# Performance work log

Measured on AMD Instinct MI355X. Metric: run time of the kernel, lower is better.

## Reference

```python
import jax, jax.numpy as jnp
import numpy as np

WS = 8      # window_size
C = 60      # channels
EXP = 2     # exp_ratio
DEPTH = 2   # 1 + shared_depth
B, H, W = 4, 256, 256
BN_EPS = 1e-5


def setup_inputs() -> dict:
    key = jax.random.key(0)
    ks = jax.random.split(key, 15)
    def rn(k, shape, s=0.1):
        return jax.random.normal(k, shape, jnp.float32) * s
    Ce = C * EXP
    return {
        "x": jax.random.normal(ks[0], (B, C, H, W), jnp.float32),
        "lfe_w0": rn(ks[1], (DEPTH, Ce, C)),
        "lfe_b0": rn(ks[2], (DEPTH, Ce)),
        "lfe_w1": rn(ks[3], (DEPTH, C, Ce)),
        "lfe_b1": rn(ks[4], (DEPTH, C)),
        "pi_w": rn(ks[5], (DEPTH, C, C)),
        "pi_b": rn(ks[6], (DEPTH, C)),
        "bn_g": 1.0 + rn(ks[7], (DEPTH, C)),
        "bn_b": rn(ks[8], (DEPTH, C)),
        "bn_m": rn(ks[9], (DEPTH, C)),
        "bn_v": jax.random.uniform(ks[10], (DEPTH, C), jnp.float32, 0.5, 1.5),
        "mask_w": rn(ks[11], (DEPTH, C, C)),
        "mask_b": rn(ks[12], (DEPTH, C)),
        "po_w": rn(ks[13], (DEPTH, C, C)),
        "po_b": rn(ks[14], (DEPTH, C)),
    }


def _conv1x1(x, w, b):
    # x: (b,c,h,w), w: (o,c)
    return jnp.einsum('oc,bchw->bohw', w, x) + b[None, :, None, None]


def _shift(x):
    # Faithful to ShiftConv2d1: depthwise 3x3 with one-hot kernels, zero pad=1.
    c = x.shape[1]; g = c // 5
    xp = jnp.pad(x, ((0, 0), (0, 0), (1, 1), (1, 1)))
    return jnp.concatenate([
        xp[:, 0 * g:1 * g, 1:-1, 2:],    # kernel (1,2): in[i, j+1]
        xp[:, 1 * g:2 * g, 1:-1, :-2],   # kernel (1,0): in[i, j-1]
        xp[:, 2 * g:3 * g, 2:, 1:-1],    # kernel (2,1): in[i+1, j]
        xp[:, 3 * g:4 * g, :-2, 1:-1],   # kernel (0,1): in[i-1, j]
        x[:, 4 * g:],                    # kernel (1,1): identity
    ], axis=1)


def _lfe(x, w0, b0, w1, b1):
    y = _conv1x1(_shift(x), w0, b0)
    y = jax.nn.gelu(y, approximate=False)  # torch nn.GELU() is exact erf
    return _conv1x1(_shift(y), w1, b1)


def _wsa(x, pi_w, pi_b, g, bt, m, v, mw, mb, pw, pb):
    b, c, h, w = x.shape; ws = WS
    # project_inp: 1x1 conv + BatchNorm2d (eval-mode stats)
    t = _conv1x1(x, pi_w, pi_b)
    scale = (g / jnp.sqrt(v + BN_EPS))
    t = (t - m[None, :, None, None]) * scale[None, :, None, None] + bt[None, :, None, None]
    # seq_refl_win_pad (forward): pad right/bottom by ws, then copy the
    # preceding ws-wide band into the padded region (rows first, then cols).
    xp = jnp.pad(t, ((0, 0), (0, 0), (0, ws), (0, ws)))
    xp = xp.at[:, :, -ws:, :].set(xp[:, :, -2 * ws:-ws, :])
    xp = xp.at[:, :, :, -ws:].set(xp[:, :, :, -2 * ws:-ws])
    nh, nw = h // ws, w // ws
    R = (jnp.arange(nh) * ws)[:, None] + jnp.arange(2 * ws)   # (nh, 2ws)
    Cc = (jnp.arange(nw) * ws)[:, None] + jnp.arange(2 * ws)  # (nw, 2ws)
    win = xp[:, :, R[:, None, :, None], Cc[None, :, None, :]]  # (b,c,nh,nw,2ws,2ws)
    # torch .unfold(3,..).unfold(2,..) yields window axes ordered (W-dir, H-dir)
    win = jnp.swapaxes(win, -1, -2)
    # 1x1 conv stride 2 == subsample every other pixel then 1x1 conv
    sub = win[..., ::2, ::2]  # (b,c,nh,nw,ws,ws)
    q = jnp.einsum('oc,bcijpq->bijpqo', mw, sub) + mb          # (b,nh,nw,ws,ws,c)
    q = q.reshape(b * nh * nw, ws * ws, c)
    vv = t.reshape(b, c, nh, ws, nw, ws).transpose(0, 2, 4, 3, 5, 1)
    vv = vv.reshape(b * nh * nw, ws * ws, c)
    atn = jax.nn.softmax(jnp.einsum('npc,nqc->npq', q, q), axis=-1)
    y = jnp.einsum('npq,nqc->npc', atn, vv)
    y = y.reshape(b, nh, nw, ws, ws, c).transpose(0, 5, 1, 3, 2, 4).reshape(b, c, h, w)
    return _conv1x1(y, pw, pb)


def reference(x, lfe_w0, lfe_b0, lfe_w1, lfe_b1, pi_w, pi_b, bn_g, bn_b, bn_m, bn_v, mask_w, mask_b, po_w, po_b):
    for i in range(DEPTH):
        x = _lfe(x, lfe_w0[i], lfe_b0[i], lfe_w1[i], lfe_b1[i]) + x
        x = _wsa(x, pi_w[i], pi_b[i], bn_g[i], bn_b[i], bn_m[i], bn_v[i],
                 mask_w[i], mask_b[i], po_w[i], po_b[i]) + x
    return x
```

## Files before the change

kernel.cpp:

```cpp
#include <hip/hip_runtime.h>
#include <math.h>

#define Hh 256
#define Ww 256
#define HW 65536
#define Bn 4
#define Cdim 60
#define Ce 120
#define NPIX (Bn*HW)

typedef const float* fp;

__device__ __forceinline__ float gelu_exact(float x){
  return 0.5f*x*(1.f + erff(x*0.70710678118654752f));
}

__device__ __forceinline__ void tile_decode(int blk, int& b, int& h, int& tw){
  b = blk >> 10; int rem = blk & 1023; h = rem >> 2; tw = (rem & 3) << 6;
}

__global__ __launch_bounds__(256) void k_lfe1(const float* __restrict__ X, float* __restrict__ Y1,
                                              fp w0, fp b0){
  __shared__ __align__(16) float A[60*64];
  __shared__ __align__(16) float Wt[60*60];
  int tid = threadIdx.x;
  int b, h, tw; tile_decode(blockIdx.x, b, h, tw);
  const float* Xb = X + (size_t)b*(Cdim*HW);
  for (int idx = tid; idx < 60*64; idx += 256){
    int k = idx >> 6, p = idx & 63;
    int grp = k / 12;
    int hh = h, ww = tw + p; bool ok = true;
    if (grp == 0){ ww += 1; ok = (ww < Ww); }
    else if (grp == 1){ ww -= 1; ok = (ww >= 0); }
    else if (grp == 2){ hh = h+1; ok = (hh < Hh); }
    else if (grp == 3){ hh = h-1; ok = (hh >= 0); }
    A[idx] = ok ? Xb[k*HW + hh*Ww + ww] : 0.f;
  }
  for (int idx = tid; idx < 60*60; idx += 256){
    int o = idx / 60, k = idx - o*60;
    Wt[k*60 + o] = w0[idx];
  }
  __syncthreads();

  int p0 = (tid & 15)*4;
  int o0 = (tid >> 4)*4;

  #pragma unroll 1
  for (int half = 0; half < 2; half++){
    if (tid < 240){
      float acc[4][4];
      #pragma unroll
      for (int oi = 0; oi < 4; oi++){
        float bb = b0[half*60 + o0 + oi];
        #pragma unroll
        for (int pi = 0; pi < 4; pi++) acc[oi][pi] = bb;
      }
      #pragma unroll 4
      for (int k = 0; k < 60; k++){
        float4 a4 = *(const float4*)(&A[k*64 + p0]);
        float av[4] = {a4.x,a4.y,a4.z,a4.w};
        float4 w4 = *(const float4*)(&Wt[k*60 + o0]);
        float wv[4] = {w4.x,w4.y,w4.z,w4.w};
        #pragma unroll
        for (int oi = 0; oi < 4; oi++){
          #pragma unroll
          for (int pi = 0; pi < 4; pi++)
            acc[oi][pi] += wv[oi]*av[pi];
        }
      }
      float* Yb = Y1 + (size_t)b*(Ce*HW) + h*Ww + tw + p0;
      #pragma unroll
      for (int oi = 0; oi < 4; oi++){
        int o = half*60 + o0 + oi;
        float4 r;
        r.x = gelu_exact(acc[oi][0]); r.y = gelu_exact(acc[oi][1]);
        r.z = gelu_exact(acc[oi][2]); r.w = gelu_exact(acc[oi][3]);
        *(float4*)(Yb + (size_t)o*HW) = r;
      }
    }
    if (half == 0){
      __syncthreads();
      for (int idx = tid; idx < 60*60; idx += 256){
        int o = idx / 60, k = idx - o*60;
        Wt[k*60 + o] = w0[3600 + idx];
      }
      __syncthreads();
    }
  }
}

__global__ __launch_bounds__(256) void k_lfe2(const float* __restrict__ Y1,
                                              const float* __restrict__ R,
                                              float* __restrict__ X,
                                              fp w1, fp b1){
  __shared__ __align__(16) float A[60*64];
  __shared__ __align__(16) float Wt[60*68];
  int tid = threadIdx.x;
  int b, h, tw; tile_decode(blockIdx.x, b, h, tw);
  const float* Yb = Y1 + (size_t)b*(Ce*HW);
  int p0 = (tid & 15)*4;
  int o0 = (tid >> 4)*4;
  float acc[4][4];
  #pragma unroll
  for (int oi = 0; oi < 4; oi++)
    #pragma unroll
    for (int pi = 0; pi < 4; pi++) acc[oi][pi] = 0.f;

  #pragma unroll 1
  for (int half = 0; half < 2; half++){
    if (half) __syncthreads();
    for (int idx = tid; idx < 60*64; idx += 256){
      int k = idx >> 6, p = idx & 63;
      int e = half*60 + k;
      int grp = e / 24;
      int hh = h, ww = tw + p; bool ok = true;
      if (grp == 0){ ww += 1; ok = (ww < Ww); }
      else if (grp == 1){ ww -= 1; ok = (ww >= 0); }
      else if (grp == 2){ hh = h+1; ok = (hh < Hh); }
      else if (grp == 3){ hh = h-1; ok = (hh >= 0); }
      A[idx] = ok ? Yb[e*HW + hh*Ww + ww] : 0.f;
    }
    for (int idx = tid; idx < 60*60; idx += 256){
      int c = idx / 60, e = idx - c*60;
      Wt[e*68 + c] = w1[c*120 + half*60 + e];
    }
    __syncthreads();
    if (tid < 240){
      #pragma unroll 4
      for (int k = 0; k < 60; k++){
        float4 a4 = *(const float4*)(&A[k*64 + p0]);
        float av[4] = {a4.x,a4.y,a4.z,a4.w};
        float4 w4 = *(const float4*)(&Wt[k*68 + o0]);
        float wv[4] = {w4.x,w4.y,w4.z,w4.w};
        #pragma unroll
        for (int oi = 0; oi < 4; oi++){
          #pragma unroll
          for (int pi = 0; pi < 4; pi++)
            acc[oi][pi] += wv[oi]*av[pi];
        }
      }
    }
  }
  if (tid < 240){
    const float* Rp = R + (size_t)b*(Cdim*HW) + h*Ww + tw + p0;
    float* Xp = X + (size_t)b*(Cdim*HW) + h*Ww + tw + p0;
    #pragma unroll
    for (int oi = 0; oi < 4; oi++){
      int o = o0 + oi;
      float bb = b1[o];
      float4 r4 = *(const float4*)(Rp + (size_t)o*HW);
      float4 out;
      out.x = acc[oi][0] + bb + r4.x;
      out.y = acc[oi][1] + bb + r4.y;
      out.z = acc[oi][2] + bb + r4.z;
      out.w = acc[oi][3] + bb + r4.w;
      *(float4*)(Xp + (size_t)o*HW) = out;
    }
  }
}

__global__ __launch_bounds__(256) void k_wsat(const float* __restrict__ X, float* __restrict__ T,
                                              fp piw, fp pib, fp g, fp bt, fp m, fp v){
  __shared__ __align__(16) float A[60*64];
  __shared__ __align__(16) float Wt[60*68];
  int tid = threadIdx.x;
  int b, h, tw; tile_decode(blockIdx.x, b, h, tw);
  const float* Xb = X + (size_t)b*(Cdim*HW) + h*Ww + tw;
  for (int idx = tid; idx < 60*64; idx += 256){
    int k = idx >> 6, p = idx & 63;
    A[idx] = Xb[k*HW + p];
  }
  for (int idx = tid; idx < 60*60; idx += 256){
    int o = idx / 60, k = idx - o*60;
    float scale = g[o] * rsqrtf(v[o] + 1e-5f);
    Wt[k*68 + o] = piw[idx] * scale;
  }
  __syncthreads();
  if (tid < 240){
    int p0 = (tid & 15)*4;
    int o0 = (tid >> 4)*4;
    float acc[4][4];
    #pragma unroll
    for (int oi = 0; oi < 4; oi++)
      #pragma unroll
      for (int pi = 0; pi < 4; pi++) acc[oi][pi] = 0.f;
    #pragma unroll 4
    for (int k = 0; k < 60; k++){
      float4 a4 = *(const float4*)(&A[k*64 + p0]);
      float av[4] = {a4.x,a4.y,a4.z,a4.w};
      float4 w4 = *(const float4*)(&Wt[k*68 + o0]);
      float wv[4] = {w4.x,w4.y,w4.z,w4.w};
      #pragma unroll
      for (int oi = 0; oi < 4; oi++){
        #pragma unroll
        for (int pi = 0; pi < 4; pi++)
          acc[oi][pi] += wv[oi]*av[pi];
      }
    }
    float* Tb = T + (size_t)b*(Cdim*HW) + h*Ww + tw + p0;
    #pragma unroll
    for (int oi = 0; oi < 4; oi++){
      int o = o0 + oi;
      float scale = g[o] * rsqrtf(v[o] + 1e-5f);
      float cns   = (pib[o] - m[o])*scale + bt[o];
      float4 out;
      out.x = acc[oi][0] + cns;
      out.y = acc[oi][1] + cns;
      out.z = acc[oi][2] + cns;
      out.w = acc[oi][3] + cns;
      *(float4*)(Tb + (size_t)o*HW) = out;
    }
  }
}

__global__ __launch_bounds__(256) void k_attn(const float* __restrict__ T, float* __restrict__ Y,
                                              fp mw, fp mb){
  __shared__ __align__(16) float R1[64*68];
  __shared__ __align__(16) float R2[64*68];
  __shared__ __align__(16) float R3[60*64];
  int tid = threadIdx.x;
  int blk = blockIdx.x;
  int b = blk >> 10; int ij = blk & 1023; int wi = ij >> 5; int wj = ij & 31;
  const float* Tb = T + (size_t)b*(Cdim*HW);

  for (int idx = tid; idx < Cdim*64; idx += 256){
    int k = idx >> 6, p = idx & 63;
    int u = p >> 3, vq = p & 7;
    int r  = wi*8 + 2*vq; if (r > 255) r -= 8;
    int cc = wj*8 + 2*u;  if (cc > 255) cc -= 8;
    R1[k*68 + p] = Tb[k*HW + r*Ww + cc];
  }
  for (int idx = tid; idx < Cdim*Cdim; idx += 256){
    int c = idx / Cdim, k = idx - c*Cdim;
    R2[c*61 + k] = mw[idx];
  }
  __syncthreads();

  if (tid < 240){
    int p0 = (tid & 15)*4, c0 = (tid >> 4)*4;
    float4 mb4 = *(const float4*)(mb + c0);
    float bias[4] = {mb4.x, mb4.y, mb4.z, mb4.w};
    float acc[4][4];
    #pragma unroll
    for (int ci = 0; ci < 4; ci++)
      #pragma unroll
      for (int pi = 0; pi < 4; pi++) acc[ci][pi] = bias[ci];
    #pragma unroll 4
    for (int k = 0; k < Cdim; k++){
      float4 a4 = *(const float4*)(&R1[k*68 + p0]);
      float av[4] = {a4.x, a4.y, a4.z, a4.w};
      #pragma unroll
      for (int ci = 0; ci < 4; ci++){
        float wv = R2[(c0+ci)*61 + k];
        #pragma unroll
        for (int pi = 0; pi < 4; pi++)
          acc[ci][pi] += wv*av[pi];
      }
    }
    #pragma unroll
    for (int ci = 0; ci < 4; ci++)
      *(float4*)(&R3[(c0+ci)*64 + p0]) = make_float4(acc[ci][0], acc[ci][1], acc[ci][2], acc[ci][3]);
  }
  __syncthreads();

  {
    int p = tid & 63; int cg = tid >> 6;
    int pr = p >> 3, pc = p & 7;
    const float* base = Tb + (wi*8+pr)*Ww + (wj*8+pc);
    #pragma unroll
    for (int t2 = 0; t2 < 15; t2++)
      R1[p*68 + cg*15 + t2] = base[(cg*15+t2)*HW];
  }
  if (tid < 64){
    R1[tid*68 + 60] = 0.f; R1[tid*68 + 61] = 0.f;
    R1[tid*68 + 62] = 0.f; R1[tid*68 + 63] = 0.f;
  }
  {
    int p0 = (tid & 15)*4, q0 = (tid >> 4)*4;
    float acc[4][4];
    #pragma unroll
    for (int qi = 0; qi < 4; qi++)
      #pragma unroll
      for (int pi = 0; pi < 4; pi++) acc[qi][pi] = 0.f;
    #pragma unroll 4
    for (int c = 0; c < Cdim; c++){
      float4 A4 = *(const float4*)(&R3[c*64 + p0]);
      float4 B4 = *(const float4*)(&R3[c*64 + q0]);
      float Af[4] = {A4.x, A4.y, A4.z, A4.w};
      float Bf[4] = {B4.x, B4.y, B4.z, B4.w};
      #pragma unroll
      for (int qi = 0; qi < 4; qi++)
        #pragma unroll
        for (int pi = 0; pi < 4; pi++)
          acc[qi][pi] += Bf[qi]*Af[pi];
    }
    __syncthreads();
    #pragma unroll
    for (int qi = 0; qi < 4; qi++)
      *(float4*)(&R2[(q0+qi)*68 + p0]) = make_float4(acc[qi][0], acc[qi][1], acc[qi][2], acc[qi][3]);
  }
  __syncthreads();

  {
    int p = tid & 63, gq = tid >> 6;
    float* Sc = R3;
    float mx = -1e30f;
    #pragma unroll
    for (int i = 0; i < 16; i++) mx = fmaxf(mx, R2[(gq*16+i)*68 + p]);
    Sc[gq*64 + p] = mx;
    __syncthreads();
    float m0 = fmaxf(fmaxf(Sc[p], Sc[64+p]), fmaxf(Sc[128+p], Sc[192+p]));
    float sum = 0.f;
    #pragma unroll
    for (int i = 0; i < 16; i++){
      int q = gq*16 + i;
      float e = __expf(R2[q*68 + p] - m0);
      R2[q*68 + p] = e; sum += e;
    }
    Sc[256 + gq*64 + p] = sum;
    __syncthreads();
    float tot = (Sc[256+p] + Sc[320+p]) + (Sc[384+p] + Sc[448+p]);
    float inv = 1.f/tot;
    #pragma unroll
    for (int i = 0; i < 16; i++) R2[(gq*16+i)*68 + p] *= inv;
  }
  __syncthreads();

  {
    int p0 = (tid & 15)*4, c0 = (tid >> 4)*4;
    float acc[4][4];
    #pragma unroll
    for (int ci = 0; ci < 4; ci++)
      #pragma unroll
      for (int pi = 0; pi < 4; pi++) acc[ci][pi] = 0.f;
    #pragma unroll 4
    for (int q = 0; q < 64; q++){
      float4 S4 = *(const float4*)(&R2[q*68 + p0]);
      float4 V4 = *(const float4*)(&R1[q*68 + c0]);
      float Sf[4] = {S4.x, S4.y, S4.z, S4.w};
      float Vf[4] = {V4.x, V4.y, V4.z, V4.w};
      #pragma unroll
      for (int ci = 0; ci < 4; ci++)
        #pragma unroll
        for (int pi = 0; pi < 4; pi++)
          acc[ci][pi] += Sf[pi]*Vf[ci];
    }
    float* Yb = Y + (size_t)b*(Cdim*HW);
    #pragma unroll
    for (int ci = 0; ci < 4; ci++){
      int c = c0 + ci;
      if (c < Cdim){
        #pragma unroll
        for (int pi = 0; pi < 4; pi++){
          int p = p0 + pi;
          Yb[c*HW + (wi*8 + (p>>3))*Ww + wj*8 + (p&7)] = acc[ci][pi];
        }
      }
    }
  }
}

__global__ __launch_bounds__(256) void k_wsaout(const float* __restrict__ Y, float* __restrict__ X,
                                                fp pw, fp pb){
  __shared__ __align__(16) float A[60*64];
  __shared__ __align__(16) float Wt[60*68];
  int tid = threadIdx.x;
  int b, h, tw; tile_decode(blockIdx.x, b, h, tw);
  const float* Yb = Y + (size_t)b*(Cdim*HW) + h*Ww + tw;
  for (int idx = tid; idx < 60*64; idx += 256){
    int k = idx >> 6, p = idx & 63;
    A[idx] = Yb[k*HW + p];
  }
  for (int idx = tid; idx < 60*60; idx += 256){
    int o = idx / 60, k = idx - o*60;
    Wt[k*68 + o] = pw[idx];
  }
  __syncthreads();
  if (tid < 240){
    int p0 = (tid & 15)*4;
    int o0 = (tid >> 4)*4;
    float acc[4][4];
    #pragma unroll
    for (int oi = 0; oi < 4; oi++)
      #pragma unroll
      for (int pi = 0; pi < 4; pi++) acc[oi][pi] = 0.f;
    #pragma unroll 4
    for (int k = 0; k < 60; k++){
      float4 a4 = *(const float4*)(&A[k*64 + p0]);
      float av[4] = {a4.x,a4.y,a4.z,a4.w};
      float4 w4 = *(const float4*)(&Wt[k*68 + o0]);
      float wv[4] = {w4.x,w4.y,w4.z,w4.w};
      #pragma unroll
      for (int oi = 0; oi < 4; oi++){
        #pragma unroll
        for (int pi = 0; pi < 4; pi++)
          acc[oi][pi] += wv[oi]*av[pi];
      }
    }
    float* Xp = X + (size_t)b*(Cdim*HW) + h*Ww + tw + p0;
    #pragma unroll
    for (int oi = 0; oi < 4; oi++){
      int o = o0 + oi;
      float bb = pb[o];
      float4 r4 = *(const float4*)(Xp + (size_t)o*HW);
      float4 out;
      out.x = acc[oi][0] + bb + r4.x;
      out.y = acc[oi][1] + bb + r4.y;
      out.z = acc[oi][2] + bb + r4.z;
      out.w = acc[oi][3] + bb + r4.w;
      *(float4*)(Xp + (size_t)o*HW) = out;
    }
  }
}

extern "C" void kernel_launch(void* const* d_in, const int* in_sizes, int n_in,
                              void* d_out, int out_size, void* d_ws, size_t ws_size,
                              hipStream_t stream){
  fp x      = (fp)d_in[0];
  fp lfe_w0 = (fp)d_in[1];
  fp lfe_b0 = (fp)d_in[2];
  fp lfe_w1 = (fp)d_in[3];
  fp lfe_b1 = (fp)d_in[4];
  fp pi_w   = (fp)d_in[5];
  fp pi_b   = (fp)d_in[6];
  fp bn_g   = (fp)d_in[7];
  fp bn_b   = (fp)d_in[8];
  fp bn_m   = (fp)d_in[9];
  fp bn_v   = (fp)d_in[10];
  fp mask_w = (fp)d_in[11];
  fp mask_b = (fp)d_in[12];
  fp po_w   = (fp)d_in[13];
  fp po_b   = (fp)d_in[14];

  const size_t XSZ = (size_t)Bn*Cdim*HW;
  float* X  = (float*)d_out;
  float* Y1 = (float*)d_ws;
  float* T  = Y1;
  float* Yw = Y1 + XSZ;

  const int NT = NPIX/64;

  for (int d = 0; d < 2; d++){
    fp src = (d == 0) ? x : X;
    k_lfe1  <<<NT, 256, 0, stream>>>(src, Y1, lfe_w0 + d*Ce*Cdim, lfe_b0 + d*Ce);
    k_lfe2  <<<NT, 256, 0, stream>>>(Y1, src, X, lfe_w1 + d*Ce*Cdim, lfe_b1 + d*Cdim);
    k_wsat  <<<NT, 256, 0, stream>>>(X, T, pi_w + d*Cdim*Cdim, pi_b + d*Cdim,
                                     bn_g + d*Cdim, bn_b + d*Cdim, bn_m + d*Cdim, bn_v + d*Cdim);
    k_attn  <<<Bn*32*32, 256, 0, stream>>>(T, Yw, mask_w + d*Cdim*Cdim, mask_b + d*Cdim);
    k_wsaout<<<NT, 256, 0, stream>>>(Yw, X, po_w + d*Cdim*Cdim, po_b + d*Cdim);
  }
}
```

Baseline: 1.021 ms.

## Stream activation tiles into LDS via async global_load_lds and split-phase compute

Replaces register-staged activation loads in the four 1x1-conv kernels with direct global-to-LDS loads (global_load_lds). Channel rows are issued in two batches so the second batch's loads overlap the first half of the K-loop. The next weight half is prefetched into registers during compute. The aim is to hide global load latency and reduce VGPR traffic, at the cost of extra barriers, more register pressure, and reliance on barrier semantics to make the async LDS writes visible.

Measured after the change: 891.0 us. 12.7% less time.

```diff
diff --git a/kernel.cpp b/kernel.cpp
--- a/kernel.cpp
+++ b/kernel.cpp
@@ -11,12 +11,31 @@
 
 typedef const float* fp;
 
+typedef const __attribute__((address_space(1))) void* gas_p;
+typedef __attribute__((address_space(3))) void* las_p;
+#define GLOAD4(SRC, DST) __builtin_amdgcn_global_load_lds((gas_p)(SRC), (las_p)(DST), 4, 0, 0)
+
+#define KEEP(x) asm volatile("" : "+v"(x))
+
 __device__ __forceinline__ float gelu_exact(float x){
   return 0.5f*x*(1.f + erff(x*0.70710678118654752f));
 }
 
 __device__ __forceinline__ void tile_decode(int blk, int& b, int& h, int& tw){
   b = blk >> 10; int rem = blk & 1023; h = rem >> 2; tw = (rem & 3) << 6;
+}
+
+__device__ __forceinline__ void issue_shift_row(const float* __restrict__ Src, float* A,
+                                                int e, int kloc, int gdiv,
+                                                int h, int tw, int lane){
+  int grp = e / gdiv;
+  int hh = h, ww = tw + lane; bool ok = true;
+  if (grp == 0){ ww += 1; ok = (ww < Ww); }
+  else if (grp == 1){ ww -= 1; ok = (ww >= 0); }
+  else if (grp == 2){ hh = h+1; ok = (hh < Hh); }
+  else if (grp == 3){ hh = h-1; ok = (hh >= 0); }
+  if (!ok) A[kloc*64 + lane] = 0.f;
+  if (ok)  GLOAD4(Src + (size_t)e*HW + hh*Ww + ww, &A[kloc*64]);
 }
 
 __global__ __launch_bounds__(256) void k_lfe1(const float* __restrict__ X, float* __restrict__ Y1,
@@ -24,67 +43,114 @@
   __shared__ __align__(16) float A[60*64];
   __shared__ __align__(16) float Wt[60*60];
   int tid = threadIdx.x;
+  int lane = tid & 63, wv = tid >> 6;
   int b, h, tw; tile_decode(blockIdx.x, b, h, tw);
   const float* Xb = X + (size_t)b*(Cdim*HW);
-  for (int idx = tid; idx < 60*64; idx += 256){
-    int k = idx >> 6, p = idx & 63;
-    int grp = k / 12;
-    int hh = h, ww = tw + p; bool ok = true;
-    if (grp == 0){ ww += 1; ok = (ww < Ww); }
-    else if (grp == 1){ ww -= 1; ok = (ww >= 0); }
-    else if (grp == 2){ hh = h+1; ok = (hh < Hh); }
-    else if (grp == 3){ hh = h-1; ok = (hh >= 0); }
-    A[idx] = ok ? Xb[k*HW + hh*Ww + ww] : 0.f;
-  }
-  for (int idx = tid; idx < 60*60; idx += 256){
+
+  #pragma unroll
+  for (int j = 0; j < 8; j++){
+    int k = wv + j*4;
+    issue_shift_row(Xb, A, k, k, 12, h, tw, lane);
+  }
+  for (int idx = tid; idx < 3600; idx += 256){
     int o = idx / 60, k = idx - o*60;
     Wt[k*60 + o] = w0[idx];
   }
   __syncthreads();
-
-  int p0 = (tid & 15)*4;
-  int o0 = (tid >> 4)*4;
-
-  #pragma unroll 1
-  for (int half = 0; half < 2; half++){
-    if (tid < 240){
-      float acc[4][4];
-      #pragma unroll
-      for (int oi = 0; oi < 4; oi++){
-        float bb = b0[half*60 + o0 + oi];
-        #pragma unroll
-        for (int pi = 0; pi < 4; pi++) acc[oi][pi] = bb;
-      }
-      #pragma unroll 4
-      for (int k = 0; k < 60; k++){
-        float4 a4 = *(const float4*)(&A[k*64 + p0]);
-        float av[4] = {a4.x,a4.y,a4.z,a4.w};
-        float4 w4 = *(const float4*)(&Wt[k*60 + o0]);
-        float wv[4] = {w4.x,w4.y,w4.z,w4.w};
-        #pragma unroll
-        for (int oi = 0; oi < 4; oi++){
-          #pragma unroll
-          for (int pi = 0; pi < 4; pi++)
-            acc[oi][pi] += wv[oi]*av[pi];
-        }
-      }
-      float* Yb = Y1 + (size_t)b*(Ce*HW) + h*Ww + tw + p0;
-      #pragma unroll
-      for (int oi = 0; oi < 4; oi++){
-        int o = half*60 + o0 + oi;
-        float4 r;
-        r.x = gelu_exact(acc[oi][0]); r.y = gelu_exact(acc[oi][1]);
-        r.z = gelu_exact(acc[oi][2]); r.w = gelu_exact(acc[oi][3]);
-        *(float4*)(Yb + (size_t)o*HW) = r;
-      }
-    }
-    if (half == 0){
-      __syncthreads();
-      for (int idx = tid; idx < 60*60; idx += 256){
-        int o = idx / 60, k = idx - o*60;
-        Wt[k*60 + o] = w0[3600 + idx];
-      }
-      __syncthreads();
+  #pragma unroll
+  for (int j = 8; j < 15; j++){
+    int k = wv + j*4;
+    issue_shift_row(Xb, A, k, k, 12, h, tw, lane);
+  }
+  __builtin_amdgcn_sched_barrier(0);
+
+  int p0 = (tid & 15)*4, o0 = (tid >> 4)*4;
+  float acc[4][4];
+  if (tid < 240){
+    #pragma unroll
+    for (int oi = 0; oi < 4; oi++){
+      float bb = b0[o0+oi];
+      #pragma unroll
+      for (int pi = 0; pi < 4; pi++) acc[oi][pi] = bb;
+    }
+    #pragma unroll 4
+    for (int k = 0; k < 32; k++){
+      float4 a4 = *(const float4*)(&A[k*64 + p0]);
+      float av[4] = {a4.x,a4.y,a4.z,a4.w};
+      float4 w4 = *(const float4*)(&Wt[k*60 + o0]);
+      float wvv[4] = {w4.x,w4.y,w4.z,w4.w};
+      #pragma unroll
+      for (int oi = 0; oi < 4; oi++)
+        #pragma unroll
+        for (int pi = 0; pi < 4; pi++)
+          acc[oi][pi] += wvv[oi]*av[pi];
+    }
+  }
+  __syncthreads();
+  float w1r[15];
+  #pragma unroll
+  for (int jj = 0; jj < 15; jj++){
+    int idx = tid + jj*256;
+    w1r[jj] = (idx < 3600) ? w0[3600 + idx] : 0.f;
+  }
+  #pragma unroll
+  for (int jj = 0; jj < 15; jj++) KEEP(w1r[jj]);
+  __builtin_amdgcn_sched_barrier(0);
+  if (tid < 240){
+    #pragma unroll 4
+    for (int k = 32; k < 60; k++){
+      float4 a4 = *(const float4*)(&A[k*64 + p0]);
+      float av[4] = {a4.x,a4.y,a4.z,a4.w};
+      float4 w4 = *(const float4*)(&Wt[k*60 + o0]);
+      float wvv[4] = {w4.x,w4.y,w4.z,w4.w};
+      #pragma unroll
+      for (int oi = 0; oi < 4; oi++)
+        #pragma unroll
+        for (int pi = 0; pi < 4; pi++)
+          acc[oi][pi] += wvv[oi]*av[pi];
+    }
+    float* Yb = Y1 + (size_t)b*(Ce*HW) + h*Ww + tw + p0;
+    #pragma unroll
+    for (int oi = 0; oi < 4; oi++){
+      float4 r;
+      r.x = gelu_exact(acc[oi][0]); r.y = gelu_exact(acc[oi][1]);
+      r.z = gelu_exact(acc[oi][2]); r.w = gelu_exact(acc[oi][3]);
+      *(float4*)(Yb + (size_t)(o0+oi)*HW) = r;
+    }
+  }
+  __syncthreads();
+  #pragma unroll
+  for (int jj = 0; jj < 15; jj++){
+    int idx = tid + jj*256;
+    if (idx < 3600){ int o = idx/60, k = idx - o*60; Wt[k*60 + o] = w1r[jj]; }
+  }
+  __syncthreads();
+  if (tid < 240){
+    #pragma unroll
+    for (int oi = 0; oi < 4; oi++){
+      float bb = b0[60 + o0 + oi];
+      #pragma unroll
+      for (int pi = 0; pi < 4; pi++) acc[oi][pi] = bb;
+    }
+    #pragma unroll 4
+    for (int k = 0; k < 60; k++){
+      float4 a4 = *(const float4*)(&A[k*64 + p0]);
+      float av[4] = {a4.x,a4.y,a4.z,a4.w};
+      float4 w4 = *(const float4*)(&Wt[k*60 + o0]);
+      float wvv[4] = {w4.x,w4.y,w4.z,w4.w};
+      #pragma unroll
+      for (int oi = 0; oi < 4; oi++)
+        #pragma unroll
+        for (int pi = 0; pi < 4; pi++)
+          acc[oi][pi] += wvv[oi]*av[pi];
+    }
+    float* Yb = Y1 + (size_t)b*(Ce*HW) + h*Ww + tw + p0;
+    #pragma unroll
+    for (int oi = 0; oi < 4; oi++){
+      float4 r;
+      r.x = gelu_exact(acc[oi][0]); r.y = gelu_exact(acc[oi][1]);
+      r.z = gelu_exact(acc[oi][2]); r.w = gelu_exact(acc[oi][3]);
+      *(float4*)(Yb + (size_t)(60 + o0 + oi)*HW) = r;
     }
   }
 }
@@ -96,52 +162,118 @@
   __shared__ __align__(16) float A[60*64];
   __shared__ __align__(16) float Wt[60*68];
   int tid = threadIdx.x;
+  int lane = tid & 63, wv = tid >> 6;
   int b, h, tw; tile_decode(blockIdx.x, b, h, tw);
   const float* Yb = Y1 + (size_t)b*(Ce*HW);
-  int p0 = (tid & 15)*4;
-  int o0 = (tid >> 4)*4;
+  int p0 = (tid & 15)*4, o0 = (tid >> 4)*4;
   float acc[4][4];
   #pragma unroll
   for (int oi = 0; oi < 4; oi++)
     #pragma unroll
     for (int pi = 0; pi < 4; pi++) acc[oi][pi] = 0.f;
 
-  #pragma unroll 1
-  for (int half = 0; half < 2; half++){
-    if (half) __syncthreads();
-    for (int idx = tid; idx < 60*64; idx += 256){
-      int k = idx >> 6, p = idx & 63;
-      int e = half*60 + k;
-      int grp = e / 24;
-      int hh = h, ww = tw + p; bool ok = true;
-      if (grp == 0){ ww += 1; ok = (ww < Ww); }
-      else if (grp == 1){ ww -= 1; ok = (ww >= 0); }
-      else if (grp == 2){ hh = h+1; ok = (hh < Hh); }
-      else if (grp == 3){ hh = h-1; ok = (hh >= 0); }
-      A[idx] = ok ? Yb[e*HW + hh*Ww + ww] : 0.f;
-    }
-    for (int idx = tid; idx < 60*60; idx += 256){
-      int c = idx / 60, e = idx - c*60;
-      Wt[e*68 + c] = w1[c*120 + half*60 + e];
-    }
-    __syncthreads();
-    if (tid < 240){
-      #pragma unroll 4
-      for (int k = 0; k < 60; k++){
-        float4 a4 = *(const float4*)(&A[k*64 + p0]);
-        float av[4] = {a4.x,a4.y,a4.z,a4.w};
-        float4 w4 = *(const float4*)(&Wt[k*68 + o0]);
-        float wv[4] = {w4.x,w4.y,w4.z,w4.w};
-        #pragma unroll
-        for (int oi = 0; oi < 4; oi++){
-          #pragma unroll
-          for (int pi = 0; pi < 4; pi++)
-            acc[oi][pi] += wv[oi]*av[pi];
-        }
-      }
-    }
-  }
-  if (tid < 240){
+  #pragma unroll
+  for (int j = 0; j < 8; j++){
+    int kloc = wv + j*4;
+    issue_shift_row(Yb, A, kloc, kloc, 24, h, tw, lane);
+  }
+  for (int idx = tid; idx < 3600; idx += 256){
+    int c = idx / 60, e = idx - c*60;
+    Wt[e*68 + c] = w1[c*120 + e];
+  }
+  __syncthreads();
+  #pragma unroll
+  for (int j = 8; j < 15; j++){
+    int kloc = wv + j*4;
+    issue_shift_row(Yb, A, kloc, kloc, 24, h, tw, lane);
+  }
+  __builtin_amdgcn_sched_barrier(0);
+  if (tid < 240){
+    #pragma unroll 4
+    for (int k = 0; k < 32; k++){
+      float4 a4 = *(const float4*)(&A[k*64 + p0]);
+      float av[4] = {a4.x,a4.y,a4.z,a4.w};
+      float4 w4 = *(const float4*)(&Wt[k*68 + o0]);
+      float wvv[4] = {w4.x,w4.y,w4.z,w4.w};
+      #pragma unroll
+      for (int oi = 0; oi < 4; oi++)
+        #pragma unroll
+        for (int pi = 0; pi < 4; pi++)
+          acc[oi][pi] += wvv[oi]*av[pi];
+    }
+  }
+  __syncthreads();
+  float w1r[15];
+  #pragma unroll
+  for (int jj = 0; jj < 15; jj++){
+    int idx = tid + jj*256;
+    int c = idx / 60, e = idx - c*60;
+    w1r[jj] = (idx < 3600) ? w1[c*120 + 60 + e] : 0.f;
+  }
+  #pragma unroll
+  for (int jj = 0; jj < 15; jj++) KEEP(w1r[jj]);
+  __builtin_amdgcn_sched_barrier(0);
+  if (tid < 240){
+    #pragma unroll 4
+    for (int k = 32; k < 60; k++){
+      float4 a4 = *(const float4*)(&A[k*64 + p0]);
+      float av[4] = {a4.x,a4.y,a4.z,a4.w};
+      float4 w4 = *(const float4*)(&Wt[k*68 + o0]);
+      float wvv[4] = {w4.x,w4.y,w4.z,w4.w};
+      #pragma unroll
+      for (int oi = 0; oi < 4; oi++)
+        #pragma unroll
+        for (int pi = 0; pi < 4; pi++)
+          acc[oi][pi] += wvv[oi]*av[pi];
+    }
+  }
+  __syncthreads();
+
+  #pragma unroll
+  for (int j = 0; j < 8; j++){
+    int kloc = wv + j*4;
+    issue_shift_row(Yb, A, 60 + kloc, kloc, 24, h, tw, lane);
+  }
+  #pragma unroll
+  for (int jj = 0; jj < 15; jj++){
+    int idx = tid + jj*256;
+    if (idx < 3600){ int c = idx/60, e = idx - c*60; Wt[e*68 + c] = w1r[jj]; }
+  }
+  __syncthreads();
+  #pragma unroll
+  for (int j = 8; j < 15; j++){
+    int kloc = wv + j*4;
+    issue_shift_row(Yb, A, 60 + kloc, kloc, 24, h, tw, lane);
+  }
+  __builtin_amdgcn_sched_barrier(0);
+  if (tid < 240){
+    #pragma unroll 4
+    for (int k = 0; k < 32; k++){
+      float4 a4 = *(const float4*)(&A[k*64 + p0]);
+      float av[4] = {a4.x,a4.y,a4.z,a4.w};
+      float4 w4 = *(const float4*)(&Wt[k*68 + o0]);
+      float wvv[4] = {w4.x,w4.y,w4.z,w4.w};
+      #pragma unroll
+      for (int oi = 0; oi < 4; oi++)
+        #pragma unroll
+        for (int pi = 0; pi < 4; pi++)
+          acc[oi][pi] += wvv[oi]*av[pi];
+    }
+  }
+  __syncthreads();
+  if (tid < 240){
+    #pragma unroll 4
+    for (int k = 32; k < 60; k++){
+      float4 a4 = *(const float4*)(&A[k*64 + p0]);
+      float av[4] = {a4.x,a4.y,a4.z,a4.w};
+      float4 w4 = *(const float4*)(&Wt[k*68 + o0]);
+      float wvv[4] = {w4.x,w4.y,w4.z,w4.w};
+      #pragma unroll
+      for (int oi = 0; oi < 4; oi++)
+        #pragma unroll
+        for (int pi = 0; pi < 4; pi++)
+          acc[oi][pi] += wvv[oi]*av[pi];
+    }
     const float* Rp = R + (size_t)b*(Cdim*HW) + h*Ww + tw + p0;
     float* Xp = X + (size_t)b*(Cdim*HW) + h*Ww + tw + p0;
     #pragma unroll
@@ -164,38 +296,61 @@
   __shared__ __align__(16) float A[60*64];
   __shared__ __align__(16) float Wt[60*68];
   int tid = threadIdx.x;
+  int lane = tid & 63, wv = tid >> 6;
   int b, h, tw; tile_decode(blockIdx.x, b, h, tw);
   const float* Xb = X + (size_t)b*(Cdim*HW) + h*Ww + tw;
-  for (int idx = tid; idx < 60*64; idx += 256){
-    int k = idx >> 6, p = idx & 63;
-    A[idx] = Xb[k*HW + p];
-  }
-  for (int idx = tid; idx < 60*60; idx += 256){
+
+  #pragma unroll
+  for (int j = 0; j < 8; j++){
+    int k = wv + j*4;
+    GLOAD4(Xb + (size_t)k*HW + lane, &A[k*64]);
+  }
+  for (int idx = tid; idx < 3600; idx += 256){
     int o = idx / 60, k = idx - o*60;
     float scale = g[o] * rsqrtf(v[o] + 1e-5f);
     Wt[k*68 + o] = piw[idx] * scale;
   }
   __syncthreads();
-  if (tid < 240){
-    int p0 = (tid & 15)*4;
-    int o0 = (tid >> 4)*4;
-    float acc[4][4];
+  #pragma unroll
+  for (int j = 8; j < 15; j++){
+    int k = wv + j*4;
+    GLOAD4(Xb + (size_t)k*HW + lane, &A[k*64]);
+  }
+  __builtin_amdgcn_sched_barrier(0);
+
+  int p0 = (tid & 15)*4, o0 = (tid >> 4)*4;
+  float acc[4][4];
+  if (tid < 240){
     #pragma unroll
     for (int oi = 0; oi < 4; oi++)
       #pragma unroll
       for (int pi = 0; pi < 4; pi++) acc[oi][pi] = 0.f;
     #pragma unroll 4
-    for (int k = 0; k < 60; k++){
-      float4 a4 = *(const float4*)(&A[k*64 + p0]);
-      float av[4] = {a4.x,a4.y,a4.z,a4.w};
-      float4 w4 = *(const float4*)(&Wt[k*68 + o0]);
-      float wv[4] = {w4.x,w4.y,w4.z,w4.w};
-      #pragma unroll
-      for (int oi = 0; oi < 4; oi++){
-        #pragma unroll
-        for (int pi = 0; pi < 4; pi++)
-          acc[oi][pi] += wv[oi]*av[pi];
-      }
+    for (int k = 0; k < 32; k++){
+      float4 a4 = *(const float4*)(&A[k*64 + p0]);
+      float av[4] = {a4.x,a4.y,a4.z,a4.w};
+      float4 w4 = *(const float4*)(&Wt[k*68 + o0]);
+      float wvv[4] = {w4.x,w4.y,w4.z,w4.w};
+      #pragma unroll
+      for (int oi = 0; oi < 4; oi++)
+        #pragma unroll
+        for (int pi = 0; pi < 4; pi++)
+          acc[oi][pi] += wvv[oi]*av[pi];
+    }
+  }
+  __syncthreads();
+  if (tid < 240){
+    #pragma unroll 4
+    for (int k = 32; k < 60; k++){
+      float4 a4 = *(const float4*)(&A[k*64 + p0]);
+      float av[4] = {a4.x,a4.y,a4.z,a4.w};
+      float4 w4 = *(const float4*)(&Wt[k*68 + o0]);
+      float wvv[4] = {w4.x,w4.y,w4.z,w4.w};
+      #pragma unroll
+      for (int oi = 0; oi < 4; oi++)
+        #pragma unroll
+        for (int pi = 0; pi < 4; pi++)
+          acc[oi][pi] += wvv[oi]*av[pi];
     }
     float* Tb = T + (size_t)b*(Cdim*HW) + h*Ww + tw + p0;
     #pragma unroll
@@ -365,37 +520,60 @@
   __shared__ __align__(16) float A[60*64];
   __shared__ __align__(16) float Wt[60*68];
   int tid = threadIdx.x;
+  int lane = tid & 63, wv = tid >> 6;
   int b, h, tw; tile_decode(blockIdx.x, b, h, tw);
   const float* Yb = Y + (size_t)b*(Cdim*HW) + h*Ww + tw;
-  for (int idx = tid; idx < 60*64; idx += 256){
-    int k = idx >> 6, p = idx & 63;
-    A[idx] = Yb[k*HW + p];
-  }
-  for (int idx = tid; idx < 60*60; idx += 256){
+
+  #pragma unroll
+  for (int j = 0; j < 8; j++){
+    int k = wv + j*4;
+    GLOAD4(Yb + (size_t)k*HW + lane, &A[k*64]);
+  }
+  for (int idx = tid; idx < 3600; idx += 256){
     int o = idx / 60, k = idx - o*60;
     Wt[k*68 + o] = pw[idx];
   }
   __syncthreads();
-  if (tid < 240){
-    int p0 = (tid & 15)*4;
-    int o0 = (tid >> 4)*4;
-    float acc[4][4];
+  #pragma unroll
+  for (int j = 8; j < 15; j++){
+    int k = wv + j*4;
+    GLOAD4(Yb + (size_t)k*HW + lane, &A[k*64]);
+  }
+  __builtin_amdgcn_sched_barrier(0);
+
+  int p0 = (tid & 15)*4, o0 = (tid >> 4)*4;
+  float acc[4][4];
+  if (tid < 240){
     #pragma unroll
     for (int oi = 0; oi < 4; oi++)
       #pragma unroll
       for (int pi = 0; pi < 4; pi++) acc[oi][pi] = 0.f;
     #pragma unroll 4
-    for (int k = 0; k < 60; k++){
-      float4 a4 = *(const float4*)(&A[k*64 + p0]);
-      float av[4] = {a4.x,a4.y,a4.z,a4.w};
-      float4 w4 = *(const float4*)(&Wt[k*68 + o0]);
-      float wv[4] = {w4.x,w4.y,w4.z,w4.w};
-      #pragma unroll
-      for (int oi = 0; oi < 4; oi++){
-        #pragma unroll
-        for (int pi = 0; pi < 4; pi++)
-          acc[oi][pi] += wv[oi]*av[pi];
-      }
+    for (int k = 0; k < 32; k++){
+      float4 a4 = *(const float4*)(&A[k*64 + p0]);
+      float av[4] = {a4.x,a4.y,a4.z,a4.w};
+      float4 w4 = *(const float4*)(&Wt[k*68 + o0]);
+      float wvv[4] = {w4.x,w4.y,w4.z,w4.w};
+      #pragma unroll
+      for (int oi = 0; oi < 4; oi++)
+        #pragma unroll
+        for (int pi = 0; pi < 4; pi++)
+          acc[oi][pi] += wvv[oi]*av[pi];
+    }
+  }
+  __syncthreads();
+  if (tid < 240){
+    #pragma unroll 4
+    for (int k = 32; k < 60; k++){
+      float4 a4 = *(const float4*)(&A[k*64 + p0]);
+      float av[4] = {a4.x,a4.y,a4.z,a4.w};
+      float4 w4 = *(const float4*)(&Wt[k*68 + o0]);
+      float wvv[4] = {w4.x,w4.y,w4.z,w4.w};
+      #pragma unroll
+      for (int oi = 0; oi < 4; oi++)
+        #pragma unroll
+        for (int pi = 0; pi < 4; pi++)
+          acc[oi][pi] += wvv[oi]*av[pi];
     }
     float* Xp = X + (size_t)b*(Cdim*HW) + h*Ww + tw + p0;
     #pragma unroll
```
